# Kernel tuning notes

Hardware: AMD Instinct MI355X
Metric: run time of the kernel (lower is better)

The kernel has to match this reference:

```python
import math
import jax, jax.numpy as jnp
import numpy as np

D_Q, D_K, D_ATT = 512, 512, 128
BSZ, NUM_Q, NUM_K = 2, 256, 2048


def setup_inputs() -> dict:
    key = jax.random.key(0)
    ks = jax.random.split(key, 12)
    s_in = 1.0 / math.sqrt(D_Q)
    s_att = 1.0 / math.sqrt(D_ATT)
    return {
        "query": jax.random.normal(ks[0], (BSZ, NUM_Q, D_Q), jnp.float32),
        "key": jax.random.normal(ks[1], (BSZ, NUM_K, D_K), jnp.float32),
        # bilinear path weights (stored [in, out])
        "W_bq": jax.random.normal(ks[2], (D_Q, D_ATT), jnp.float32) * s_in,
        "b_bq": jax.random.normal(ks[3], (D_ATT,), jnp.float32) * s_in,
        "W_bk": jax.random.normal(ks[4], (D_K, D_ATT), jnp.float32) * s_in,
        "b_bk": jax.random.normal(ks[5], (D_ATT,), jnp.float32) * s_in,
        # linear (additive) path weights
        "W_lq": jax.random.normal(ks[6], (D_Q, D_ATT), jnp.float32) * s_in,
        "b_lq": jax.random.normal(ks[7], (D_ATT,), jnp.float32) * s_in,
        "W_lk": jax.random.normal(ks[8], (D_K, D_ATT), jnp.float32) * s_in,
        "b_lk": jax.random.normal(ks[9], (D_ATT,), jnp.float32) * s_in,
        # final projection to scalar logit
        "v_att": jax.random.normal(ks[10], (D_ATT,), jnp.float32) * s_att,
        "b_att": jax.random.normal(ks[11], (), jnp.float32) * s_att,
    }


def reference(query, key, W_bq, b_bq, W_bk, b_bk, W_lq, b_lq, W_lk, b_lk, v_att, b_att):
    # type_att = 3: linear (additive Bahdanau) + low-rank bilinear
    # --- linear path: v^T tanh(W'[q;k] + b) ---
    ql = query @ W_lq + b_lq                       # [b, q, d]
    kl = key @ W_lk + b_lk                         # [b, k, d]
    hidden = jnp.tanh(ql[:, :, None, :] + kl[:, None, :, :])  # [b, q, k, d]
    lin_logits = jnp.einsum('bqkd,d->bqk', hidden, v_att) + b_att
    # --- bilinear path: (q^T U)(V^T k) / sqrt(d) ---
    qb = query @ W_bq + b_bq                       # [b, q, d]
    kb = key @ W_bk + b_bk                         # [b, k, d]
    bi_logits = jnp.einsum('bqd,bkd->bqk', qb, kb) / math.sqrt(D_ATT)
    return lin_logits + bi_logits
```

## Files before the change

### kernel.cpp

```cpp
#include <hip/hip_runtime.h>
#include <hip/hip_bf16.h>
#include <cstdint>

#define DEV_INLINE __device__ __forceinline__

typedef __attribute__((ext_vector_type(8))) short short8v;
typedef __attribute__((ext_vector_type(4))) float f32x4;
typedef __attribute__((ext_vector_type(2))) float v2f;

constexpr int BSZ = 2, NUM_Q = 256, NUM_K = 2048, D_IN = 512, D_ATT = 128;
constexpr float S_ATT = 0.08838834764831845f;
constexpr float C2 = 2.8853900817779268f;

DEV_INLINE uint16_t f2bf(float f) {
  uint32_t u = __float_as_uint(f);
  return (uint16_t)((u + 0x7fffu + ((u >> 16) & 1u)) >> 16);
}

DEV_INLINE float fast_exp2(float x) {
#if __has_builtin(__builtin_amdgcn_exp2f)
  return __builtin_amdgcn_exp2f(x);
#else
  return __expf(0.6931471805599453f * x);
#endif
}

__global__ __launch_bounds__(256) void pack_w(
    const float* __restrict__ Wlq, const float* __restrict__ Wbq,
    const float* __restrict__ Wlk, const float* __restrict__ Wbk,
    const float* __restrict__ v_att, const float* __restrict__ b_att,
    uint16_t* __restrict__ Wt2, float* __restrict__ vsumc) {
  __shared__ float xs[256 * 17];
  const int bid = blockIdx.x;
  const int t = threadIdx.x;

  const int mat = bid >> 5, cb = (bid >> 1) & 15, kh = bid & 1;
  const float* W = (mat == 0) ? (cb < 8 ? Wlq : Wbq) : (cb < 8 ? Wlk : Wbk);
  const int cbase = (cb & 7) * 16;

#pragma unroll
  for (int i = 0; i < 4; ++i) {
    const int fq = t + i * 256;
    const int k = fq >> 2, c4 = (fq & 3) * 4;
    const float4 v = *(const float4*)&W[(size_t)(kh * 256 + k) * D_ATT + cbase + c4];
    xs[k * 17 + c4 + 0] = v.x;
    xs[k * 17 + c4 + 1] = v.y;
    xs[k * 17 + c4 + 2] = v.z;
    xs[k * 17 + c4 + 3] = v.w;
  }
  __syncthreads();

#pragma unroll
  for (int i = 0; i < 2; ++i) {
    const int e = t + i * 256;
    const int sl = e >> 6, l = e & 63;
    const int kb_ = sl * 32 + (l >> 4) * 8;
    const int c = l & 15;
    uint16_t o[8];
#pragma unroll
    for (int j = 0; j < 8; ++j) o[j] = f2bf(xs[(kb_ + j) * 17 + c]);
    const int sg = kh * 8 + sl;
    *(uint4*)(Wt2 + ((size_t)(mat * 16 + cb) * 16 + sg) * 512 + l * 8) =
        *(const uint4*)o;
  }

  if (bid == 0 && t < 64) {
    float s = v_att[t] + v_att[t + 64];
#pragma unroll
    for (int off = 32; off >= 1; off >>= 1) s += __shfl_down(s, off);
    if (t == 0) vsumc[0] = s + b_att[0];
  }
}

__global__ __launch_bounds__(256) void proj_gemm(
    const float* __restrict__ Xq, const float* __restrict__ Xk,
    const uint16_t* __restrict__ Wt2,
    const float* __restrict__ b_lq, const float* __restrict__ b_bq,
    const float* __restrict__ b_lk, const float* __restrict__ b_bk,
    float* __restrict__ eq, uint16_t* __restrict__ qb,
    uint16_t* __restrict__ ek, uint16_t* __restrict__ kb) {
  __shared__ __align__(16) unsigned char alds[16 * 1024];
  const int bid = blockIdx.x;
  const int t = threadIdx.x;
  const int l = t & 63;
  const int rt = bid >> 1;
  const int ct2 = (bid & 1) * 4 + (t >> 6);

  const bool isq = rt < 32;
  const int mat = isq ? 0 : 1;
  const int row0 = isq ? rt * 16 : (rt - 32) * 16;
  const float* src = (isq ? Xq : Xk) + (size_t)row0 * D_IN;

#pragma unroll
  for (int i = 0; i < 4; ++i) {
    const int f = t + i * 256;
    const int row = f >> 6, c = f & 63;
    const float* s8 = src + (size_t)row * D_IN + c * 8;
    const float4 a = *(const float4*)s8;
    const float4 b = *(const float4*)(s8 + 4);
    uint16_t o[8];
    o[0] = f2bf(a.x); o[1] = f2bf(a.y); o[2] = f2bf(a.z); o[3] = f2bf(a.w);
    o[4] = f2bf(b.x); o[5] = f2bf(b.y); o[6] = f2bf(b.z); o[7] = f2bf(b.w);
    *(uint4*)(alds + row * 1024 + ((c ^ (row & 7)) << 4)) = *(const uint4*)o;
  }
  __syncthreads();

  const uint16_t* wbase =
      Wt2 + ((size_t)(mat * 16 + ct2 * 2) * 16) * 512 + l * 8;
  const int arow = l & 15;

  f32x4 acc0 = {0.f, 0.f, 0.f, 0.f}, acc1 = {0.f, 0.f, 0.f, 0.f};
#pragma unroll 4
  for (int s = 0; s < 16; ++s) {
    const int chunk = (s * 4 + (l >> 4)) ^ (arow & 7);
    const short8v a = *(const short8v*)(alds + arow * 1024 + (chunk << 4));
    const short8v b0 = *(const short8v*)(wbase + (size_t)s * 512);
    const short8v b1 = *(const short8v*)(wbase + (size_t)(16 + s) * 512);
    acc0 = __builtin_amdgcn_mfma_f32_16x16x32_bf16(a, b0, acc0, 0, 0, 0);
    acc1 = __builtin_amdgcn_mfma_f32_16x16x32_bf16(a, b1, acc1, 0, 0, 0);
  }

  const int lrow4 = (l >> 4) * 4;
#pragma unroll
  for (int half = 0; half < 2; ++half) {
    const f32x4 acc = half ? acc1 : acc0;
    const int cbb = ct2 * 32 + half * 16;
    const int cl = (cbb + (l & 15)) & 127;
    float bias;
    if (isq) bias = (cbb < 128) ? b_lq[cl] : b_bq[cl];
    else     bias = (cbb < 128) ? b_lk[cl] : b_bk[cl];
#pragma unroll
    for (int jr = 0; jr < 4; ++jr) {
      const int row = row0 + lrow4 + jr;
      const float val = acc[jr] + bias;
      if (isq) {
        if (cbb < 128) eq[row * D_ATT + cl] = fast_exp2(C2 * val);
        else           qb[row * D_ATT + cl] = f2bf(val * S_ATT);
      } else {
        if (cbb < 128) ek[row * D_ATT + cl] = f2bf(fast_exp2(C2 * val));
        else           kb[row * D_ATT + cl] = f2bf(val);
      }
    }
  }
}

__global__ __launch_bounds__(256) void fused_kernel(
    const float* __restrict__ eq_g, const uint16_t* __restrict__ qb_g,
    const uint16_t* __restrict__ ek_g, const uint16_t* __restrict__ kb_g,
    const float* __restrict__ v_att, const float* __restrict__ vsumc,
    float* __restrict__ out) {
  __shared__ __align__(16) unsigned char klds[64 * 256];
  __shared__ float vlds[D_ATT];
  __shared__ float sblds[16 * 64];

  const int tid = threadIdx.x;
  const int b = blockIdx.x >> 9;
  const int qt = (blockIdx.x >> 5) & 15;
  const int kt = blockIdx.x & 31;

  const uint4* ekg = (const uint4*)(ek_g + (size_t)(b * NUM_K + kt * 64) * D_ATT);
#pragma unroll
  for (int i = 0; i < 4; ++i) {
    const int f = tid + i * 256;
    const int kr = f >> 4, c = f & 15;
    *(uint4*)(klds + kr * 256 + ((c ^ (kr & 7)) << 4)) = ekg[f];
  }
  if (tid < 32) {
    float4 t = ((const float4*)v_att)[tid];
    t.x *= -2.f; t.y *= -2.f; t.z *= -2.f; t.w *= -2.f;
    ((float4*)vlds)[tid] = t;
  }

  {
    const int l = tid & 63;
    const int w = tid >> 6;
    const uint16_t* ap =
        qb_g + (size_t)(b * NUM_Q + qt * 16 + (l & 15)) * D_ATT + (l >> 4) * 8;
    const uint16_t* bp =
        kb_g + (size_t)(b * NUM_K + kt * 64 + w * 16 + (l & 15)) * D_ATT + (l >> 4) * 8;
    f32x4 acc = {0.f, 0.f, 0.f, 0.f};
#pragma unroll
    for (int s = 0; s < 4; ++s) {
      const short8v a = *(const short8v*)(ap + s * 32);
      const short8v bb = *(const short8v*)(bp + s * 32);
      acc = __builtin_amdgcn_mfma_f32_16x16x32_bf16(a, bb, acc, 0, 0, 0);
    }
    const int col = w * 16 + (l & 15);
    const int r0 = (l >> 4) * 4;
#pragma unroll
    for (int jr = 0; jr < 4; ++jr) sblds[(r0 + jr) * 64 + col] = acc[jr];
  }
  __syncthreads();

  const int k = tid & 63;
  const int w = tid >> 6;
  const int qoff =
      __builtin_amdgcn_readfirstlane((b * NUM_Q + qt * 16 + (tid >> 6) * 4) * D_ATT);
  const float* qbase = eq_g + qoff;

  const v2f one2 = {1.0f, 1.0f};
  v2f accp[4];
#pragma unroll
  for (int qq = 0; qq < 4; ++qq) accp[qq] = (v2f){0.f, 0.f};

  for (int d0 = 0; d0 < D_ATT; d0 += 8) {
    const int c = d0 >> 3;
    const uint4 ekv = *(const uint4*)(klds + k * 256 + ((c ^ (k & 7)) << 4));
    v2f ek2[4];
    ek2[0] = (v2f){__uint_as_float(ekv.x << 16), __uint_as_float(ekv.x & 0xffff0000u)};
    ek2[1] = (v2f){__uint_as_float(ekv.y << 16), __uint_as_float(ekv.y & 0xffff0000u)};
    ek2[2] = (v2f){__uint_as_float(ekv.z << 16), __uint_as_float(ekv.z & 0xffff0000u)};
    ek2[3] = (v2f){__uint_as_float(ekv.w << 16), __uint_as_float(ekv.w & 0xffff0000u)};
    v2f vv2[4];
#pragma unroll
    for (int p = 0; p < 4; ++p)
      vv2[p] = *(const v2f*)&vlds[d0 + p * 2];
#pragma unroll
    for (int qq = 0; qq < 4; ++qq) {
      const float4 e0 = *(const float4*)(qbase + qq * D_ATT + d0);
      const float4 e1 = *(const float4*)(qbase + qq * D_ATT + d0 + 4);
      v2f dd0 = __builtin_elementwise_fma((v2f){e0.x, e0.y}, ek2[0], one2);
      v2f dd1 = __builtin_elementwise_fma((v2f){e0.z, e0.w}, ek2[1], one2);
      v2f dd2 = __builtin_elementwise_fma((v2f){e1.x, e1.y}, ek2[2], one2);
      v2f dd3 = __builtin_elementwise_fma((v2f){e1.z, e1.w}, ek2[3], one2);
      {
        const v2f P = dd0 * dd1;
        const float r = __builtin_amdgcn_rcpf(P.x * P.y);
        const v2f t = (v2f){r, r} * (v2f){P.y, P.x};
        accp[qq] = __builtin_elementwise_fma(vv2[0], t * dd1, accp[qq]);
        accp[qq] = __builtin_elementwise_fma(vv2[1], t * dd0, accp[qq]);
      }
      {
        const v2f P = dd2 * dd3;
        const float r = __builtin_amdgcn_rcpf(P.x * P.y);
        const v2f t = (v2f){r, r} * (v2f){P.y, P.x};
        accp[qq] = __builtin_elementwise_fma(vv2[2], t * dd3, accp[qq]);
        accp[qq] = __builtin_elementwise_fma(vv2[3], t * dd2, accp[qq]);
      }
    }
  }

  const float cst = vsumc[0];
#pragma unroll
  for (int qq = 0; qq < 4; ++qq) {
    const int q = qt * 16 + w * 4 + qq;
    out[(size_t)(b * NUM_Q + q) * NUM_K + kt * 64 + k] =
        accp[qq].x + accp[qq].y + sblds[(w * 4 + qq) * 64 + k] + cst;
  }
}

extern "C" void kernel_launch(void* const* d_in, const int* in_sizes, int n_in,
                              void* d_out, int out_size, void* d_ws, size_t ws_size,
                              hipStream_t stream) {
  const float* query = (const float*)d_in[0];
  const float* key   = (const float*)d_in[1];
  const float* W_bq  = (const float*)d_in[2];
  const float* b_bq  = (const float*)d_in[3];
  const float* W_bk  = (const float*)d_in[4];
  const float* b_bk  = (const float*)d_in[5];
  const float* W_lq  = (const float*)d_in[6];
  const float* b_lq  = (const float*)d_in[7];
  const float* W_lk  = (const float*)d_in[8];
  const float* b_lk  = (const float*)d_in[9];
  const float* v_att = (const float*)d_in[10];
  const float* b_att = (const float*)d_in[11];

  float* eq = (float*)d_ws;
  uint16_t* qb = (uint16_t*)(eq + 512 * D_ATT);
  uint16_t* ek = qb + 512 * D_ATT;
  uint16_t* kb = ek + 4096 * D_ATT;
  uint16_t* Wt2 = kb + 4096 * D_ATT;
  float* vsumc = (float*)(Wt2 + 2 * 256 * 512);

  pack_w<<<64, 256, 0, stream>>>(W_lq, W_bq, W_lk, W_bk, v_att, b_att,
                                 Wt2, vsumc);
  proj_gemm<<<576, 256, 0, stream>>>(query, key, Wt2, b_lq, b_bq, b_lk, b_bk,
                                     eq, qb, ek, kb);
  fused_kernel<<<BSZ * 16 * 32, 256, 0, stream>>>(
      eq, qb, ek, kb, v_att, vsumc, (float*)d_out);
}
```

Measured before the change: 35.57 us.

## Double block size to 512 threads in projection and fused attention kernels

The projection GEMM now runs one block per 16-row tile with 8 waves covering all 256 output columns, instead of two 4-wave blocks each loading the same A tile. This removes the duplicated fp32 load and bf16 conversion of the input rows. The fused kernel uses 8 waves per block: each wave handles 2 query rows instead of 4 in the tanh path, and the bilinear MFMA is split across two halves of the head dimension, with the partial sums added from two LDS buffers at output. This halves the per-thread serial work and adds wave-level parallelism, at the cost of fewer independent accumulators per thread and possibly lower occupancy.

```diff
diff --git a/kernel.cpp b/kernel.cpp
--- a/kernel.cpp
+++ b/kernel.cpp
@@ -72,7 +72,7 @@
   }
 }
 
-__global__ __launch_bounds__(256) void proj_gemm(
+__global__ __launch_bounds__(512) void proj_gemm(
     const float* __restrict__ Xq, const float* __restrict__ Xk,
     const uint16_t* __restrict__ Wt2,
     const float* __restrict__ b_lq, const float* __restrict__ b_bq,
@@ -80,11 +80,10 @@
     float* __restrict__ eq, uint16_t* __restrict__ qb,
     uint16_t* __restrict__ ek, uint16_t* __restrict__ kb) {
   __shared__ __align__(16) unsigned char alds[16 * 1024];
-  const int bid = blockIdx.x;
+  const int rt = blockIdx.x;
   const int t = threadIdx.x;
   const int l = t & 63;
-  const int rt = bid >> 1;
-  const int ct2 = (bid & 1) * 4 + (t >> 6);
+  const int ct2 = t >> 6;
 
   const bool isq = rt < 32;
   const int mat = isq ? 0 : 1;
@@ -92,8 +91,8 @@
   const float* src = (isq ? Xq : Xk) + (size_t)row0 * D_IN;
 
 #pragma unroll
-  for (int i = 0; i < 4; ++i) {
-    const int f = t + i * 256;
+  for (int i = 0; i < 2; ++i) {
+    const int f = t + i * 512;
     const int row = f >> 6, c = f & 63;
     const float* s8 = src + (size_t)row * D_IN + c * 8;
     const float4 a = *(const float4*)s8;
@@ -144,14 +143,14 @@
   }
 }
 
-__global__ __launch_bounds__(256) void fused_kernel(
+__global__ __launch_bounds__(512) void fused_kernel(
     const float* __restrict__ eq_g, const uint16_t* __restrict__ qb_g,
     const uint16_t* __restrict__ ek_g, const uint16_t* __restrict__ kb_g,
     const float* __restrict__ v_att, const float* __restrict__ vsumc,
     float* __restrict__ out) {
   __shared__ __align__(16) unsigned char klds[64 * 256];
   __shared__ float vlds[D_ATT];
-  __shared__ float sblds[16 * 64];
+  __shared__ float sblds[2][16 * 64];
 
   const int tid = threadIdx.x;
   const int b = blockIdx.x >> 9;
@@ -160,8 +159,8 @@
 
   const uint4* ekg = (const uint4*)(ek_g + (size_t)(b * NUM_K + kt * 64) * D_ATT);
 #pragma unroll
-  for (int i = 0; i < 4; ++i) {
-    const int f = tid + i * 256;
+  for (int i = 0; i < 2; ++i) {
+    const int f = tid + i * 512;
     const int kr = f >> 4, c = f & 15;
     *(uint4*)(klds + kr * 256 + ((c ^ (kr & 7)) << 4)) = ekg[f];
   }
@@ -174,34 +173,35 @@
   {
     const int l = tid & 63;
     const int w = tid >> 6;
-    const uint16_t* ap =
-        qb_g + (size_t)(b * NUM_Q + qt * 16 + (l & 15)) * D_ATT + (l >> 4) * 8;
-    const uint16_t* bp =
-        kb_g + (size_t)(b * NUM_K + kt * 64 + w * 16 + (l & 15)) * D_ATT + (l >> 4) * 8;
+    const int wc = w & 3, dh = w >> 2;
+    const uint16_t* ap = qb_g +
+        (size_t)(b * NUM_Q + qt * 16 + (l & 15)) * D_ATT + dh * 64 + (l >> 4) * 8;
+    const uint16_t* bp = kb_g +
+        (size_t)(b * NUM_K + kt * 64 + wc * 16 + (l & 15)) * D_ATT + dh * 64 + (l >> 4) * 8;
     f32x4 acc = {0.f, 0.f, 0.f, 0.f};
 #pragma unroll
-    for (int s = 0; s < 4; ++s) {
+    for (int s = 0; s < 2; ++s) {
       const short8v a = *(const short8v*)(ap + s * 32);
       const short8v bb = *(const short8v*)(bp + s * 32);
       acc = __builtin_amdgcn_mfma_f32_16x16x32_bf16(a, bb, acc, 0, 0, 0);
     }
-    const int col = w * 16 + (l & 15);
+    const int col = wc * 16 + (l & 15);
     const int r0 = (l >> 4) * 4;
 #pragma unroll
-    for (int jr = 0; jr < 4; ++jr) sblds[(r0 + jr) * 64 + col] = acc[jr];
+    for (int jr = 0; jr < 4; ++jr) sblds[dh][(r0 + jr) * 64 + col] = acc[jr];
   }
   __syncthreads();
 
   const int k = tid & 63;
-  const int w = tid >> 6;
+  const int qg = tid >> 6;
   const int qoff =
-      __builtin_amdgcn_readfirstlane((b * NUM_Q + qt * 16 + (tid >> 6) * 4) * D_ATT);
+      __builtin_amdgcn_readfirstlane((b * NUM_Q + qt * 16 + (tid >> 6) * 2) * D_ATT);
   const float* qbase = eq_g + qoff;
 
   const v2f one2 = {1.0f, 1.0f};
-  v2f accp[4];
-#pragma unroll
-  for (int qq = 0; qq < 4; ++qq) accp[qq] = (v2f){0.f, 0.f};
+  v2f accp[2];
+  accp[0] = (v2f){0.f, 0.f};
+  accp[1] = (v2f){0.f, 0.f};
 
   for (int d0 = 0; d0 < D_ATT; d0 += 8) {
     const int c = d0 >> 3;
@@ -216,7 +216,7 @@
     for (int p = 0; p < 4; ++p)
       vv2[p] = *(const v2f*)&vlds[d0 + p * 2];
 #pragma unroll
-    for (int qq = 0; qq < 4; ++qq) {
+    for (int qq = 0; qq < 2; ++qq) {
       const float4 e0 = *(const float4*)(qbase + qq * D_ATT + d0);
       const float4 e1 = *(const float4*)(qbase + qq * D_ATT + d0 + 4);
       v2f dd0 = __builtin_elementwise_fma((v2f){e0.x, e0.y}, ek2[0], one2);
@@ -242,10 +242,12 @@
 
   const float cst = vsumc[0];
 #pragma unroll
-  for (int qq = 0; qq < 4; ++qq) {
-    const int q = qt * 16 + w * 4 + qq;
+  for (int qq = 0; qq < 2; ++qq) {
+    const int qrow = qg * 2 + qq;
+    const int q = qt * 16 + qrow;
     out[(size_t)(b * NUM_Q + q) * NUM_K + kt * 64 + k] =
-        accp[qq].x + accp[qq].y + sblds[(w * 4 + qq) * 64 + k] + cst;
+        accp[qq].x + accp[qq].y + sblds[0][qrow * 64 + k] +
+        sblds[1][qrow * 64 + k] + cst;
   }
 }
 
@@ -274,8 +276,8 @@
 
   pack_w<<<64, 256, 0, stream>>>(W_lq, W_bq, W_lk, W_bk, v_att, b_att,
                                  Wt2, vsumc);
-  proj_gemm<<<576, 256, 0, stream>>>(query, key, Wt2, b_lq, b_bq, b_lk, b_bk,
+  proj_gemm<<<288, 512, 0, stream>>>(query, key, Wt2, b_lq, b_bq, b_lk, b_bk,
                                      eq, qb, ek, kb);
-  fused_kernel<<<BSZ * 16 * 32, 256, 0, stream>>>(
+  fused_kernel<<<BSZ * 16 * 32, 512, 0, stream>>>(
       eq, qb, ek, kb, v_att, vsumc, (float*)d_out);
 }
```

Result: slower. 37.53 us (+5.5%).
